# Performance work log

Measured on AMD Instinct MI355X. Metric: run time of the kernel, lower is better.

Reference implementation:

```python
import jax, jax.numpy as jnp
import numpy as np

jax.config.update("jax_enable_x64", True)

HLB_LVL_MAX = 20
HLB_LVL = 5
HLB_SHIFT = True
HLB_MAX = 2 ** HLB_LVL_MAX                      # 1048576
HLB_BIAS = (2 ** (HLB_LVL_MAX - HLB_LVL) - 1) if HLB_SHIFT else 0   # 32767
NUM_BITS = HLB_LVL_MAX + (1 if HLB_SHIFT else 0)  # 21 bits per axis, 63 total -> int64


def hilbert_encode3d(grd, num_bits):
    """Skilling's AxesToTranspose + bit interleave: 3D grid coords -> Hilbert order.
    grd: [..., 3] int64, coords < 2**num_bits. Returns int64 [...].
    Fixed-trip-count Python loops over bits (unrolled at trace time, ~21 iters)."""
    nd = 3
    x = [grd[..., i] for i in range(nd)]
    M = 1 << (num_bits - 1)
    # Inverse undo excess work
    Q = M
    while Q > 1:
        P = Q - 1
        for i in range(nd):
            cond = (x[i] & Q) != 0
            t = (x[0] ^ x[i]) & P
            new_x0 = jnp.where(cond, x[0] ^ P, x[0] ^ t)   # invert low bits of x0, or exchange
            new_xi = jnp.where(cond, x[i], x[i] ^ t)
            x[0] = new_x0
            if i != 0:
                x[i] = new_xi
        Q >>= 1
    # Gray encode
    for i in range(1, nd):
        x[i] = x[i] ^ x[i - 1]
    t = jnp.zeros_like(x[0])
    Q = M
    while Q > 1:
        t = jnp.where((x[nd - 1] & Q) != 0, t ^ (Q - 1), t)
        Q >>= 1
    for i in range(nd):
        x[i] = x[i] ^ t
    # Interleave bits of the transposed coords (x[0] most significant at each level)
    h = jnp.zeros_like(x[0])
    for b in range(num_bits):
        for i in range(nd):
            bit = (x[i] >> b) & 1
            h = h | (bit << (b * nd + (nd - 1 - i)))
    return h


def setup_inputs() -> dict:
    key = jax.random.key(0)
    z = jax.random.normal(key, (32, 131072, 3), dtype=jnp.float32)
    return {"z": z}


def reference(z):
    z = z.astype(jnp.float64)
    z_ce = z.mean(axis=1, keepdims=True)                                  # [B,1,3]
    r = jnp.sqrt(jnp.max(jnp.sum((z - z_ce) ** 2, axis=2), axis=1))       # [B]
    z_r = r[:, None, None] + 1e-6                                          # [B,1,1]
    z_nm = (z - z_ce + z_r) / (2.0 * z_r)                                  # normalized to ~[0,1]
    grd_idx = (HLB_MAX * z_nm).astype(jnp.int64) + HLB_BIAS                # quantize (trunc toward 0)
    hlb_ord = hilbert_encode3d(grd_idx, NUM_BITS)                          # [B,N] int64
    idx_pa = jnp.argsort(hlb_ord, axis=1)                                  # permutation along curve
    idx_re = jnp.argsort(idx_pa, axis=1)                                   # inverse permutation
    return idx_pa, idx_re
```

## Files before the change

kernel.cpp:

```cpp
#include <hip/hip_runtime.h>

typedef unsigned int u32;
typedef unsigned long long u64;
typedef unsigned short u16;

#define NB 32
#define NP 131072
#define THREADS 256
#define STHREADS 512
#define RADIX 256
#define PASSES 6

#define SBPB 32
#define STILE 4096
#define SIPT 8
#define EBPB 64
#define ETILE 2048
#define EIPT 8



__device__ __forceinline__ u64 spread3(u32 v) {
    u64 x = (u64)(v & 0x1FFFFFu);
    x = (x | (x << 32)) & 0x001F00000000FFFFull;
    x = (x | (x << 16)) & 0x001F0000FF0000FFull;
    x = (x | (x << 8))  & 0x100F00F00F00F00Full;
    x = (x | (x << 4))  & 0x10C30C30C30C30C3ull;
    x = (x | (x << 2))  & 0x1249249249249249ull;
    return x;
}

__device__ __forceinline__ u64 hilbert3d(u32 x0, u32 x1, u32 x2) {
    #pragma unroll
    for (int q = 20; q >= 3; --q) {
        u32 Q = 1u << q, P = Q - 1u;
        if (x0 & Q) x0 ^= P;
        u32 t = (x0 ^ x1) & P;
        if (x1 & Q) { x0 ^= P; } else { x0 ^= t; x1 ^= t; }
        t = (x0 ^ x2) & P;
        if (x2 & Q) { x0 ^= P; } else { x0 ^= t; x2 ^= t; }
    }
    x1 ^= x0;
    x2 ^= x1;
    u32 y = x2;
    y ^= y >> 1; y ^= y >> 2; y ^= y >> 4; y ^= y >> 8; y ^= y >> 16;
    u32 t2 = y >> 1;
    x0 ^= t2; x1 ^= t2; x2 ^= t2;
    return (spread3(x0) << 2) | (spread3(x1) << 1) | spread3(x2);
}


__global__ __launch_bounds__(THREADS) void k_sum(const float* __restrict__ z,
                                                 double* __restrict__ partial) {
    int id = blockIdx.x;
    int b = (id & 7) * 4 + ((id >> 3) >> 6);
    int blk = (id >> 3) & 63;
    int tid = threadIdx.x;
    const float* zb = z + ((size_t)b * NP + (size_t)blk * ETILE) * 3;
    double s0 = 0.0, s1 = 0.0, s2 = 0.0;
    #pragma unroll
    for (int r = 0; r < EIPT; ++r) {
        int p = r * THREADS + tid;
        s0 += (double)zb[p * 3 + 0];
        s1 += (double)zb[p * 3 + 1];
        s2 += (double)zb[p * 3 + 2];
    }
    for (int off = 32; off > 0; off >>= 1) {
        s0 += __shfl_down(s0, off);
        s1 += __shfl_down(s1, off);
        s2 += __shfl_down(s2, off);
    }
    __shared__ double red[4][3];
    int lane = tid & 63, wave = tid >> 6;
    if (lane == 0) { red[wave][0] = s0; red[wave][1] = s1; red[wave][2] = s2; }
    __syncthreads();
    if (tid == 0) {
        size_t o = ((size_t)b * EBPB + blk) * 3;
        partial[o + 0] = red[0][0] + red[1][0] + red[2][0] + red[3][0];
        partial[o + 1] = red[0][1] + red[1][1] + red[2][1] + red[3][1];
        partial[o + 2] = red[0][2] + red[1][2] + red[2][2] + red[3][2];
    }
}

__global__ __launch_bounds__(64) void k_centroid(const double* __restrict__ partial,
                                                 double* __restrict__ cent) {
    int b = blockIdx.x, lane = threadIdx.x;
    size_t o = ((size_t)b * EBPB + lane) * 3;
    double v0 = partial[o + 0], v1 = partial[o + 1], v2 = partial[o + 2];
    for (int off = 32; off > 0; off >>= 1) {
        v0 += __shfl_down(v0, off);
        v1 += __shfl_down(v1, off);
        v2 += __shfl_down(v2, off);
    }
    if (lane == 0) {
        cent[b * 4 + 0] = v0 / (double)NP;
        cent[b * 4 + 1] = v1 / (double)NP;
        cent[b * 4 + 2] = v2 / (double)NP;
    }
}

__global__ __launch_bounds__(THREADS) void k_maxp(const float* __restrict__ z,
                                                  const double* __restrict__ cent,
                                                  double* __restrict__ pmax) {
    int id = blockIdx.x;
    int b = (id & 7) * 4 + ((id >> 3) >> 6);
    int blk = (id >> 3) & 63;
    int tid = threadIdx.x;
    double c0 = cent[b * 4 + 0], c1 = cent[b * 4 + 1], c2 = cent[b * 4 + 2];
    const float* zb = z + ((size_t)b * NP + (size_t)blk * ETILE) * 3;
    double m = 0.0;
    #pragma unroll
    for (int r = 0; r < EIPT; ++r) {
        int p = r * THREADS + tid;
        double d0 = (double)zb[p * 3 + 0] - c0;
        double d1 = (double)zb[p * 3 + 1] - c1;
        double d2 = (double)zb[p * 3 + 2] - c2;
        double s = (d0 * d0 + d1 * d1) + d2 * d2;
        m = fmax(m, s);
    }
    for (int off = 32; off > 0; off >>= 1) m = fmax(m, __shfl_down(m, off));
    __shared__ double red[4];
    int lane = tid & 63, wave = tid >> 6;
    if (lane == 0) red[wave] = m;
    __syncthreads();
    if (tid == 0) pmax[(size_t)b * EBPB + blk] = fmax(fmax(red[0], red[1]), fmax(red[2], red[3]));
}

__global__ __launch_bounds__(64) void k_radius(const double* __restrict__ pmax,
                                               const double* __restrict__ cent,
                                               double* __restrict__ norm) {
    int b = blockIdx.x, lane = threadIdx.x;
    double m = pmax[(size_t)b * EBPB + lane];
    for (int off = 32; off > 0; off >>= 1) m = fmax(m, __shfl_down(m, off));
    if (lane == 0) {
        double zr = sqrt(m) + 1e-6;
        double A = 1048576.0 / (2.0 * zr);
        norm[b * 4 + 0] = A;
        norm[b * 4 + 1] = (zr - cent[b * 4 + 0]) * A;
        norm[b * 4 + 2] = (zr - cent[b * 4 + 1]) * A;
        norm[b * 4 + 3] = (zr - cent[b * 4 + 2]) * A;
    }
}


__global__ __launch_bounds__(THREADS) void k_encode(const float* __restrict__ z,
                                                    const double* __restrict__ norm,
                                                    u32* __restrict__ klo,
                                                    u32* __restrict__ khi,
                                                    u32* __restrict__ hist) {
    int id = blockIdx.x;
    int b = (id & 7) * 4 + ((id >> 3) >> 6);
    int blk = (id >> 3) & 63;
    int tid = threadIdx.x;
    __shared__ u32 lh[RADIX];
    lh[tid] = 0;
    __syncthreads();
    double A  = norm[b * 4 + 0];
    double B0 = norm[b * 4 + 1], B1 = norm[b * 4 + 2], B2 = norm[b * 4 + 3];
    size_t batchBase = (size_t)b * NP;
    for (int r = 0; r < EIPT; ++r) {
        int p = blk * ETILE + r * THREADS + tid;
        size_t zi = (batchBase + p) * 3;
        u32 g0 = (u32)fma((double)z[zi + 0], A, B0) + 32767u;
        u32 g1 = (u32)fma((double)z[zi + 1], A, B1) + 32767u;
        u32 g2 = (u32)fma((double)z[zi + 2], A, B2) + 32767u;
        u64 key = hilbert3d(g0, g1, g2) >> 16;
        u32 lo = (u32)key;
        u32 hp = ((u32)(key >> 32) << 17) | (u32)p;
        klo[batchBase + p] = lo;
        khi[batchBase + p] = hp;
        atomicAdd(&lh[lo & 255u], 1u);
    }
    __syncthreads();
    hist[((size_t)b * RADIX + tid) * EBPB + blk] = lh[tid];
}

__device__ u32 g_lut[128];

__global__ __launch_bounds__(THREADS) void k_encode2(const float* __restrict__ z,
                                                     const double* __restrict__ norm,
                                                     u32* __restrict__ klo,
                                                     u32* __restrict__ khi,
                                                     u32* __restrict__ hist) {
    int id = blockIdx.x;
    int b = (id & 7) * 4 + ((id >> 3) >> 6);
    int blk = (id >> 3) & 63;
    int tid = threadIdx.x;
    __shared__ u32 lh[RADIX];
    __shared__ u32 ltw[128];
    lh[tid] = 0;
    if (tid < 128) ltw[tid] = g_lut[tid];
    __syncthreads();
    const unsigned char* lt = (const unsigned char*)ltw;
    double A  = norm[b * 4 + 0];
    double B0 = norm[b * 4 + 1], B1 = norm[b * 4 + 2], B2 = norm[b * 4 + 3];
    size_t batchBase = (size_t)b * NP;
    #pragma unroll
    for (int rr = 0; rr < EIPT; rr += 4) {
        u32 g0[4], g1[4], g2[4];
        #pragma unroll
        for (int j = 0; j < 4; ++j) {
            int p = blk * ETILE + (rr + j) * THREADS + tid;
            size_t zi = (batchBase + p) * 3;
            g0[j] = (u32)fma((double)z[zi + 0], A, B0) + 32767u;
            g1[j] = (u32)fma((double)z[zi + 1], A, B1) + 32767u;
            g2[j] = (u32)fma((double)z[zi + 2], A, B2) + 32767u;
        }
        u32 st[4] = {0u, 0u, 0u, 0u};
        u32 Hh[4] = {0u, 0u, 0u, 0u};
        u32 Hl[4] = {0u, 0u, 0u, 0u};
        #pragma unroll
        for (int l = 20; l >= 12; --l) {
            #pragma unroll
            for (int j = 0; j < 4; ++j) {
                u32 o = (((g0[j] >> l) & 1u) << 2) | (((g1[j] >> l) & 1u) << 1)
                      | ((g2[j] >> l) & 1u);
                u32 e = (u32)lt[st[j] | o];
                Hh[j] = (Hh[j] << 3) | (e & 7u);
                st[j] = e & 0xF8u;
            }
        }
        #pragma unroll
        for (int l = 11; l >= 2; --l) {
            #pragma unroll
            for (int j = 0; j < 4; ++j) {
                u32 o = (((g0[j] >> l) & 1u) << 2) | (((g1[j] >> l) & 1u) << 1)
                      | ((g2[j] >> l) & 1u);
                u32 e = (u32)lt[st[j] | o];
                Hl[j] = (Hl[j] << 3) | (e & 7u);
                st[j] = e & 0xF8u;
            }
        }
        #pragma unroll
        for (int j = 0; j < 4; ++j) {
            int p = blk * ETILE + (rr + j) * THREADS + tid;
            u32 lo = (Hl[j] >> 10) | (Hh[j] << 20);
            u32 hp = ((Hh[j] >> 12) << 17) | (u32)p;
            klo[batchBase + p] = lo;
            khi[batchBase + p] = hp;
            atomicAdd(&lh[lo & 255u], 1u);
        }
    }
    __syncthreads();
    hist[((size_t)b * RADIX + tid) * EBPB + blk] = lh[tid];
}


__global__ __launch_bounds__(THREADS) void k_hist(const u32* __restrict__ dig,
                                                  u32* __restrict__ hist, int shift) {
    int id = blockIdx.x;
    int b = (id & 7) * 4 + ((id >> 3) >> 6);
    int blk = (id >> 3) & 63;
    int tid = threadIdx.x;
    __shared__ u32 lh[RADIX];
    lh[tid] = 0;
    __syncthreads();
    const uint4* dv = (const uint4*)(dig + (size_t)b * NP + (size_t)blk * ETILE);
    #pragma unroll
    for (int r = 0; r < EIPT / 4; ++r) {
        uint4 k = dv[r * THREADS + tid];
        atomicAdd(&lh[(k.x >> shift) & 255u], 1u);
        atomicAdd(&lh[(k.y >> shift) & 255u], 1u);
        atomicAdd(&lh[(k.z >> shift) & 255u], 1u);
        atomicAdd(&lh[(k.w >> shift) & 255u], 1u);
    }
    __syncthreads();
    hist[((size_t)b * RADIX + tid) * EBPB + blk] = lh[tid];
}


template<bool HAS_W1, bool OUT_W0, bool LAST>
__global__ __launch_bounds__(STHREADS, 8) void k_scatter(
    const u32* __restrict__ digIn,
    const u32* __restrict__ w1In,
    u32* __restrict__ w0Out, u32* __restrict__ w1Out,
    int* __restrict__ out0, int* __restrict__ out1,
    const u32* __restrict__ hist, int shiftW)
{
    int id = blockIdx.x;
    int b = (id & 7) * 4 + ((id >> 3) >> 5);
    int blk = (id >> 3) & 31;
    int tid = threadIdx.x, lane = tid & 63, wave = tid >> 6;

    __shared__ __align__(16) u32 sbuf[HAS_W1 ? 2 * STILE : STILE];
    __shared__ u16 wrun[8][RADIX];
    __shared__ u16 lstart[RADIX];
    __shared__ u32 baseS[RADIX];
    __shared__ u32 wsum[4];
    uint2* stage2 = reinterpret_cast<uint2*>(sbuf);
    u32* stage1 = sbuf;

    {
        int d2 = tid & 255, hw = (tid >> 8) * 4;
        wrun[hw + 0][d2] = 0; wrun[hw + 1][d2] = 0;
        wrun[hw + 2][d2] = 0; wrun[hw + 3][d2] = 0;
    }

    size_t batchBase = (size_t)b * NP;
    u32 tileOff = (u32)blk * STILE + (u32)wave * (STILE / 8);

    u32 w0[SIPT], w1v[SIPT], dr[SIPT];
    u64 lmask = (1ull << lane) - 1ull;

    #pragma unroll
    for (int it = 0; it < SIPT; ++it)
        w0[it] = digIn[batchBase + tileOff + it * 64 + lane];
    if (HAS_W1) {
        #pragma unroll
        for (int it = 0; it < SIPT; ++it)
            w1v[it] = w1In[batchBase + tileOff + it * 64 + lane];
    }

    u32 tot = 0, part = 0, vscan = 0;
    if (tid < 256) {
        const uint4* hp = (const uint4*)(hist + ((size_t)b * RADIX + tid) * EBPB);
        int lim = blk * 2;
        #pragma unroll
        for (int q = 0; q < EBPB / 4; ++q) {
            uint4 v = hp[q];
            int s = q * 4;
            tot += v.x + v.y + v.z + v.w;
            part += (s + 0 < lim ? v.x : 0u) + (s + 1 < lim ? v.y : 0u)
                  + (s + 2 < lim ? v.z : 0u) + (s + 3 < lim ? v.w : 0u);
        }
        vscan = tot;
        for (int off = 1; off < 64; off <<= 1) {
            u32 n = __shfl_up(vscan, off);
            if (lane >= off) vscan += n;
        }
        if (lane == 63) wsum[wave] = vscan;
    }
    __syncthreads();
    if (tid < 256) {
        u32 woff = 0;
        for (int w = 0; w < 4; ++w)
            if (w < wave) woff += wsum[w];
        baseS[tid] = woff + vscan - tot + part;
    }

    #pragma unroll
    for (int it = 0; it < SIPT; ++it) {
        u32 d = (w0[it] >> shiftW) & 255u;
        u64 m = ~0ull;
        #pragma unroll
        for (int bb = 0; bb < 8; ++bb) {
            u64 bal = __ballot((d >> bb) & 1u);
            m &= ((d >> bb) & 1u) ? bal : ~bal;
        }
        u32 lower = (u32)__popcll(m & lmask);
        u32 base = (u32)wrun[wave][d];
        if (lower == 0) wrun[wave][d] = (u16)(base + (u32)__popcll(m));
        dr[it] = (d << 16) | (base + lower);
    }
    __syncthreads();

    u32 cnt = 0, vs2 = 0;
    if (tid < 256) {
        u32 run = 0;
        #pragma unroll
        for (int w = 0; w < 8; ++w) { u32 c = wrun[w][tid]; wrun[w][tid] = (u16)run; run += c; }
        cnt = run;
        vs2 = cnt;
        for (int off = 1; off < 64; off <<= 1) {
            u32 n = __shfl_up(vs2, off);
            if (lane >= off) vs2 += n;
        }
        if (lane == 63) wsum[wave] = vs2;
    }
    __syncthreads();
    if (tid < 256) {
        u32 woff = 0;
        for (int w = 0; w < 4; ++w)
            if (w < wave) woff += wsum[w];
        lstart[tid] = (u16)(woff + vs2 - cnt);
    }
    __syncthreads();

    if (HAS_W1) {
        #pragma unroll
        for (int it = 0; it < SIPT; ++it) {
            u32 d = dr[it] >> 16, r = dr[it] & 0xFFFFu;
            u32 slot = (u32)lstart[d] + (u32)wrun[wave][d] + r;
            stage2[slot] = make_uint2(w0[it], w1v[it]);
        }
        __syncthreads();
        #pragma unroll
        for (int r = 0; r < SIPT; ++r) {
            int s = r * STHREADS + tid;
            uint2 kv = stage2[s];
            u32 d = (kv.x >> shiftW) & 255u;
            u32 pos = baseS[d] + (u32)s - (u32)lstart[d];
            if (OUT_W0) w0Out[batchBase + pos] = kv.x;
            w1Out[batchBase + pos] = kv.y;
        }
    } else {
        #pragma unroll
        for (int it = 0; it < SIPT; ++it) {
            u32 d = dr[it] >> 16, r = dr[it] & 0xFFFFu;
            u32 slot = (u32)lstart[d] + (u32)wrun[wave][d] + r;
            stage1[slot] = w0[it];
        }
        __syncthreads();
        #pragma unroll
        for (int r = 0; r < SIPT; ++r) {
            int s = r * STHREADS + tid;
            u32 k = stage1[s];
            u32 d = (k >> shiftW) & 255u;
            u32 pos = baseS[d] + (u32)s - (u32)lstart[d];
            if (LAST) {
                u32 idx = k & 0x1FFFFu;
                out0[batchBase + pos] = (int)idx;
                out1[batchBase + idx] = (int)pos;
            } else {
                w0Out[batchBase + pos] = k;
            }
        }
    }
}


namespace lut_build {

static u64 hfull(u32 a, u32 bcoord, u32 c) {
    u32 x[3] = {a, bcoord, c};
    const u32 M = 1u << 20;
    for (u32 Q = M; Q > 1; Q >>= 1) {
        u32 P = Q - 1u;
        for (int i = 0; i < 3; ++i) {
            if (x[i] & Q) x[0] ^= P;
            else { u32 t = (x[0] ^ x[i]) & P; x[0] ^= t; x[i] ^= t; }
        }
    }
    x[1] ^= x[0]; x[2] ^= x[1];
    u32 t = 0;
    for (u32 Q = M; Q > 1; Q >>= 1) if (x[2] & Q) t ^= (Q - 1u);
    x[0] ^= t; x[1] ^= t; x[2] ^= t;
    u64 h = 0;
    for (int bb = 0; bb < 21; ++bb)
        for (int i = 0; i < 3; ++i)
            h |= (u64)((x[i] >> bb) & 1u) << (bb * 3 + (2 - i));
    return h;
}

static int digit_at(u32 p0, u32 p1, u32 p2, int l) {
    return (int)((hfull(p0, p1, p2) >> (3 * l)) & 7u);
}

struct Sig { unsigned char v[72]; };

static bool sig_eq(const Sig& x, const Sig& y) {
    for (int i = 0; i < 72; ++i) if (x.v[i] != y.v[i]) return false;
    return true;
}

static void mk_sig(u32 c0, u32 c1, u32 c2, int l, Sig& s) {
    for (int o = 0; o < 8; ++o) {
        u32 p0 = c0 | ((u32)((o >> 2) & 1) << l);
        u32 p1 = c1 | ((u32)((o >> 1) & 1) << l);
        u32 p2 = c2 | ((u32)(o & 1) << l);
        s.v[o] = (unsigned char)digit_at(p0, p1, p2, l);
        for (int o2 = 0; o2 < 8; ++o2) {
            u32 q0 = p0 | ((u32)((o2 >> 2) & 1) << (l - 1));
            u32 q1 = p1 | ((u32)((o2 >> 1) & 1) << (l - 1));
            u32 q2 = p2 | ((u32)(o2 & 1) << (l - 1));
            s.v[8 + o * 8 + o2] = (unsigned char)digit_at(q0, q1, q2, l - 1);
        }
    }
}

static bool build(unsigned char* tab) {
    const int MAXS = 48;
    static Sig sigs[MAXS];
    struct Node { u32 c0, c1, c2; int l; };
    static Node nodes[MAXS];
    bool expanded[MAXS] = {false};
    int ns = 0;
    for (int i = 0; i < 512; ++i) tab[i] = 0;
    mk_sig(0, 0, 0, 20, sigs[0]);
    nodes[0] = {0, 0, 0, 20};
    ns = 1;
    bool progress = true;
    while (progress) {
        progress = false;
        for (int sI = 0; sI < ns; ++sI) {
            if (expanded[sI]) continue;
            Node n = nodes[sI];
            if (n.l < 2) return false;
            for (int o = 0; o < 8; ++o) {
                u32 p0 = n.c0 | ((u32)((o >> 2) & 1) << n.l);
                u32 p1 = n.c1 | ((u32)((o >> 1) & 1) << n.l);
                u32 p2 = n.c2 | ((u32)(o & 1) << n.l);
                int d = digit_at(p0, p1, p2, n.l);
                Sig cs; mk_sig(p0, p1, p2, n.l - 1, cs);
                int cid = -1;
                for (int k = 0; k < ns; ++k)
                    if (sig_eq(sigs[k], cs)) { cid = k; break; }
                if (cid < 0) {
                    if (ns >= MAXS) return false;
                    cid = ns;
                    sigs[ns] = cs;
                    nodes[ns] = {p0, p1, p2, n.l - 1};
                    ns++;
                }
                if (cid >= 32) return false;
                tab[sI * 8 + o] = (unsigned char)(d | (cid << 3));
            }
            expanded[sI] = true;
            progress = true;
        }
    }
    u64 rng = 0x9E3779B97F4A7C15ull;
    for (int it = 0; it < 6008; ++it) {
        u32 p0, p1, p2;
        if (it < 8) {
            p0 = (it & 4) ? 0x1FFFFFu : 0u;
            p1 = (it & 2) ? 0x1FFFFFu : 0u;
            p2 = (it & 1) ? 0x1FFFFFu : 0u;
        } else {
            rng ^= rng << 13; rng ^= rng >> 7; rng ^= rng << 17; p0 = (u32)(rng & 0x1FFFFFu);
            rng ^= rng << 13; rng ^= rng >> 7; rng ^= rng << 17; p1 = (u32)(rng & 0x1FFFFFu);
            rng ^= rng << 13; rng ^= rng >> 7; rng ^= rng << 17; p2 = (u32)(rng & 0x1FFFFFu);
        }
        u32 s8 = 0, Hh = 0, Hl = 0;
        for (int l = 20; l >= 12; --l) {
            u32 o = (((p0 >> l) & 1u) << 2) | (((p1 >> l) & 1u) << 1) | ((p2 >> l) & 1u);
            u32 e = tab[s8 | o];
            Hh = (Hh << 3) | (e & 7u);
            s8 = e & 0xF8u;
        }
        for (int l = 11; l >= 2; --l) {
            u32 o = (((p0 >> l) & 1u) << 2) | (((p1 >> l) & 1u) << 1) | ((p2 >> l) & 1u);
            u32 e = tab[s8 | o];
            Hl = (Hl << 3) | (e & 7u);
            s8 = e & 0xF8u;
        }
        u32 lo = (Hl >> 10) | (Hh << 20);
        u32 hi15 = Hh >> 12;
        u64 key = ((u64)hi15 << 32) | (u64)lo;
        if (key != (hfull(p0, p1, p2) >> 16)) return false;
    }
    return true;
}

}

static unsigned char h_tab[512];

struct LutInit {
    bool ok;
    void* dev;
    LutInit() : ok(false), dev(nullptr) {
        ok = lut_build::build(h_tab);
        if (ok) {
            if (hipGetSymbolAddress(&dev, HIP_SYMBOL(g_lut)) != hipSuccess || dev == nullptr)
                ok = false;
        }
    }
};


extern "C" void kernel_launch(void* const* d_in, const int* in_sizes, int n_in,
                              void* d_out, int out_size, void* d_ws, size_t ws_size,
                              hipStream_t stream) {
    const float* z = (const float*)d_in[0];
    int* out0 = (int*)d_out;
    int* out1 = out0 + (size_t)NB * NP;

    char* ws = (char*)d_ws;
    u32* loA  = (u32*)(ws + 0);
    u32* hiA  = (u32*)(ws + 16777216);
    u32* loB  = (u32*)(ws + 33554432);
    u32* hiB  = (u32*)(ws + 50331648);
    u32* hist = (u32*)(ws + 67108864);
    double* partial = (double*)(ws + 69206016);
    double* pmax    = (double*)(ws + 69255168);
    double* cent    = (double*)(ws + 69271552);
    double* norm    = (double*)(ws + 69272576);

    static LutInit li;

    const int egrid = NB * EBPB;
    const int sgrid = NB * SBPB;

    if (li.ok) {
        hipMemcpyAsync(li.dev, h_tab, 512, hipMemcpyHostToDevice, stream);
    }

    k_sum<<<egrid, THREADS, 0, stream>>>(z, partial);
    k_centroid<<<NB, 64, 0, stream>>>(partial, cent);
    k_maxp<<<egrid, THREADS, 0, stream>>>(z, cent, pmax);
    k_radius<<<NB, 64, 0, stream>>>(pmax, cent, norm);
    if (li.ok) {
        k_encode2<<<egrid, THREADS, 0, stream>>>(z, norm, loA, hiA, hist);
    } else {
        k_encode<<<egrid, THREADS, 0, stream>>>(z, norm, loA, hiA, hist);
    }

    k_scatter<true,  true,  false><<<sgrid, STHREADS, 0, stream>>>(
        loA, hiA, loB, hiB, nullptr, nullptr, hist, 0);
    k_hist<<<egrid, THREADS, 0, stream>>>(loB, hist, 8);
    k_scatter<true,  true,  false><<<sgrid, STHREADS, 0, stream>>>(
        loB, hiB, loA, hiA, nullptr, nullptr, hist, 8);
    k_hist<<<egrid, THREADS, 0, stream>>>(loA, hist, 16);
    k_scatter<true,  true,  false><<<sgrid, STHREADS, 0, stream>>>(
        loA, hiA, loB, hiB, nullptr, nullptr, hist, 16);
    k_hist<<<egrid, THREADS, 0, stream>>>(loB, hist, 24);
    k_scatter<true,  false, false><<<sgrid, STHREADS, 0, stream>>>(
        loB, hiB, nullptr, hiA, nullptr, nullptr, hist, 24);
    k_hist<<<egrid, THREADS, 0, stream>>>(hiA, hist, 17);
    k_scatter<false, true,  false><<<sgrid, STHREADS, 0, stream>>>(
        hiA, nullptr, hiB, nullptr, nullptr, nullptr, hist, 17);
    k_hist<<<egrid, THREADS, 0, stream>>>(hiB, hist, 25);
    k_scatter<false, false, true ><<<sgrid, STHREADS, 0, stream>>>(
        hiB, nullptr, nullptr, nullptr, out0, out1, hist, 25);
}
```

Measured before the change: 307.8 us.

## Fold centroid and radius reductions into consumers; vectorize z loads and key stores

Removes the two tiny single-wave kernels (k_centroid, k_radius). Each block of k_maxp and k_encode now recomputes the per-batch centroid and normalization from the partial sums and partial maxima in a shared-memory prologue. The z reads in k_maxp and k_encode2 switch to float4 loads that cover four points per thread, and the key stores become uint4. This saves two launches and their serialization gaps, plus some memory transactions, at the cost of redundant small reductions in every block and a different point-to-thread mapping.

```diff
diff --git a/kernel.cpp b/kernel.cpp
--- a/kernel.cpp
+++ b/kernel.cpp
@@ -11,13 +11,13 @@
 #define RADIX 256
 #define PASSES 6
 
+
 #define SBPB 32
 #define STILE 4096
 #define SIPT 8
 #define EBPB 64
 #define ETILE 2048
 #define EIPT 8
-
 
 
 __device__ __forceinline__ u64 spread3(u32 v) {
@@ -82,41 +82,47 @@
     }
 }
 
-__global__ __launch_bounds__(64) void k_centroid(const double* __restrict__ partial,
-                                                 double* __restrict__ cent) {
-    int b = blockIdx.x, lane = threadIdx.x;
-    size_t o = ((size_t)b * EBPB + lane) * 3;
-    double v0 = partial[o + 0], v1 = partial[o + 1], v2 = partial[o + 2];
-    for (int off = 32; off > 0; off >>= 1) {
-        v0 += __shfl_down(v0, off);
-        v1 += __shfl_down(v1, off);
-        v2 += __shfl_down(v2, off);
-    }
-    if (lane == 0) {
-        cent[b * 4 + 0] = v0 / (double)NP;
-        cent[b * 4 + 1] = v1 / (double)NP;
-        cent[b * 4 + 2] = v2 / (double)NP;
-    }
-}
-
 __global__ __launch_bounds__(THREADS) void k_maxp(const float* __restrict__ z,
-                                                  const double* __restrict__ cent,
+                                                  const double* __restrict__ partial,
                                                   double* __restrict__ pmax) {
     int id = blockIdx.x;
     int b = (id & 7) * 4 + ((id >> 3) >> 6);
     int blk = (id >> 3) & 63;
     int tid = threadIdx.x;
-    double c0 = cent[b * 4 + 0], c1 = cent[b * 4 + 1], c2 = cent[b * 4 + 2];
-    const float* zb = z + ((size_t)b * NP + (size_t)blk * ETILE) * 3;
+    __shared__ double cS[3];
+    if (tid < 64) {
+        size_t o = ((size_t)b * EBPB + tid) * 3;
+        double v0 = partial[o + 0], v1 = partial[o + 1], v2 = partial[o + 2];
+        for (int off = 32; off > 0; off >>= 1) {
+            v0 += __shfl_down(v0, off);
+            v1 += __shfl_down(v1, off);
+            v2 += __shfl_down(v2, off);
+        }
+        if (tid == 0) {
+            cS[0] = v0 / (double)NP;
+            cS[1] = v1 / (double)NP;
+            cS[2] = v2 / (double)NP;
+        }
+    }
+    __syncthreads();
+    double c0 = cS[0], c1 = cS[1], c2 = cS[2];
+    const float4* zb4 = (const float4*)(z + ((size_t)b * NP + (size_t)blk * ETILE) * 3);
     double m = 0.0;
     #pragma unroll
-    for (int r = 0; r < EIPT; ++r) {
-        int p = r * THREADS + tid;
-        double d0 = (double)zb[p * 3 + 0] - c0;
-        double d1 = (double)zb[p * 3 + 1] - c1;
-        double d2 = (double)zb[p * 3 + 2] - c2;
-        double s = (d0 * d0 + d1 * d1) + d2 * d2;
-        m = fmax(m, s);
+    for (int g = 0; g < 2; ++g) {
+        int q4 = g * 768 + tid * 3;
+        float4 va = zb4[q4 + 0], vb = zb4[q4 + 1], vc = zb4[q4 + 2];
+        float px[4] = {va.x, va.w, vb.z, vc.y};
+        float py[4] = {va.y, vb.x, vb.w, vc.z};
+        float pz[4] = {va.z, vb.y, vc.x, vc.w};
+        #pragma unroll
+        for (int j = 0; j < 4; ++j) {
+            double d0 = (double)px[j] - c0;
+            double d1 = (double)py[j] - c1;
+            double d2 = (double)pz[j] - c2;
+            double s = (d0 * d0 + d1 * d1) + d2 * d2;
+            m = fmax(m, s);
+        }
     }
     for (int off = 32; off > 0; off >>= 1) m = fmax(m, __shfl_down(m, off));
     __shared__ double red[4];
@@ -126,25 +132,34 @@
     if (tid == 0) pmax[(size_t)b * EBPB + blk] = fmax(fmax(red[0], red[1]), fmax(red[2], red[3]));
 }
 
-__global__ __launch_bounds__(64) void k_radius(const double* __restrict__ pmax,
-                                               const double* __restrict__ cent,
-                                               double* __restrict__ norm) {
-    int b = blockIdx.x, lane = threadIdx.x;
-    double m = pmax[(size_t)b * EBPB + lane];
-    for (int off = 32; off > 0; off >>= 1) m = fmax(m, __shfl_down(m, off));
-    if (lane == 0) {
-        double zr = sqrt(m) + 1e-6;
-        double A = 1048576.0 / (2.0 * zr);
-        norm[b * 4 + 0] = A;
-        norm[b * 4 + 1] = (zr - cent[b * 4 + 0]) * A;
-        norm[b * 4 + 2] = (zr - cent[b * 4 + 1]) * A;
-        norm[b * 4 + 3] = (zr - cent[b * 4 + 2]) * A;
-    }
-}
-
+
+__device__ __forceinline__ void quant_prologue(const double* __restrict__ partial,
+                                               const double* __restrict__ pmax,
+                                               int b, int tid, double* nS) {
+    if (tid < 64) {
+        size_t o = ((size_t)b * EBPB + tid) * 3;
+        double v0 = partial[o + 0], v1 = partial[o + 1], v2 = partial[o + 2];
+        for (int off = 32; off > 0; off >>= 1) {
+            v0 += __shfl_down(v0, off);
+            v1 += __shfl_down(v1, off);
+            v2 += __shfl_down(v2, off);
+        }
+        double m = pmax[(size_t)b * EBPB + tid];
+        for (int off = 32; off > 0; off >>= 1) m = fmax(m, __shfl_down(m, off));
+        if (tid == 0) {
+            double zr = sqrt(m) + 1e-6;
+            double A = 1048576.0 / (2.0 * zr);
+            nS[0] = A;
+            nS[1] = (zr - v0 / (double)NP) * A;
+            nS[2] = (zr - v1 / (double)NP) * A;
+            nS[3] = (zr - v2 / (double)NP) * A;
+        }
+    }
+}
 
 __global__ __launch_bounds__(THREADS) void k_encode(const float* __restrict__ z,
-                                                    const double* __restrict__ norm,
+                                                    const double* __restrict__ partial,
+                                                    const double* __restrict__ pmax,
                                                     u32* __restrict__ klo,
                                                     u32* __restrict__ khi,
                                                     u32* __restrict__ hist) {
@@ -153,10 +168,11 @@
     int blk = (id >> 3) & 63;
     int tid = threadIdx.x;
     __shared__ u32 lh[RADIX];
+    __shared__ double nS[4];
     lh[tid] = 0;
-    __syncthreads();
-    double A  = norm[b * 4 + 0];
-    double B0 = norm[b * 4 + 1], B1 = norm[b * 4 + 2], B2 = norm[b * 4 + 3];
+    quant_prologue(partial, pmax, b, tid, nS);
+    __syncthreads();
+    double A = nS[0], B0 = nS[1], B1 = nS[2], B2 = nS[3];
     size_t batchBase = (size_t)b * NP;
     for (int r = 0; r < EIPT; ++r) {
         int p = blk * ETILE + r * THREADS + tid;
@@ -178,7 +194,8 @@
 __device__ u32 g_lut[128];
 
 __global__ __launch_bounds__(THREADS) void k_encode2(const float* __restrict__ z,
-                                                     const double* __restrict__ norm,
+                                                     const double* __restrict__ partial,
+                                                     const double* __restrict__ pmax,
                                                      u32* __restrict__ klo,
                                                      u32* __restrict__ khi,
                                                      u32* __restrict__ hist) {
@@ -188,23 +205,29 @@
     int tid = threadIdx.x;
     __shared__ u32 lh[RADIX];
     __shared__ u32 ltw[128];
+    __shared__ double nS[4];
     lh[tid] = 0;
-    if (tid < 128) ltw[tid] = g_lut[tid];
+    if (tid >= 128 && tid < 256) ltw[tid - 128] = g_lut[tid - 128];
+    quant_prologue(partial, pmax, b, tid, nS);
     __syncthreads();
     const unsigned char* lt = (const unsigned char*)ltw;
-    double A  = norm[b * 4 + 0];
-    double B0 = norm[b * 4 + 1], B1 = norm[b * 4 + 2], B2 = norm[b * 4 + 3];
+    double A = nS[0], B0 = nS[1], B1 = nS[2], B2 = nS[3];
     size_t batchBase = (size_t)b * NP;
+    const float4* zb4 = (const float4*)(z + (batchBase + (size_t)blk * ETILE) * 3);
     #pragma unroll
-    for (int rr = 0; rr < EIPT; rr += 4) {
+    for (int g = 0; g < 2; ++g) {
+        int p0i = blk * ETILE + g * 1024 + tid * 4;
+        int q4 = g * 768 + tid * 3;
+        float4 va = zb4[q4 + 0], vb = zb4[q4 + 1], vc = zb4[q4 + 2];
+        float px[4] = {va.x, va.w, vb.z, vc.y};
+        float py[4] = {va.y, vb.x, vb.w, vc.z};
+        float pz[4] = {va.z, vb.y, vc.x, vc.w};
         u32 g0[4], g1[4], g2[4];
         #pragma unroll
         for (int j = 0; j < 4; ++j) {
-            int p = blk * ETILE + (rr + j) * THREADS + tid;
-            size_t zi = (batchBase + p) * 3;
-            g0[j] = (u32)fma((double)z[zi + 0], A, B0) + 32767u;
-            g1[j] = (u32)fma((double)z[zi + 1], A, B1) + 32767u;
-            g2[j] = (u32)fma((double)z[zi + 2], A, B2) + 32767u;
+            g0[j] = (u32)fma((double)px[j], A, B0) + 32767u;
+            g1[j] = (u32)fma((double)py[j], A, B1) + 32767u;
+            g2[j] = (u32)fma((double)pz[j], A, B2) + 32767u;
         }
         u32 st[4] = {0u, 0u, 0u, 0u};
         u32 Hh[4] = {0u, 0u, 0u, 0u};
@@ -231,15 +254,15 @@
                 st[j] = e & 0xF8u;
             }
         }
+        u32 lo[4], hp[4];
         #pragma unroll
         for (int j = 0; j < 4; ++j) {
-            int p = blk * ETILE + (rr + j) * THREADS + tid;
-            u32 lo = (Hl[j] >> 10) | (Hh[j] << 20);
-            u32 hp = ((Hh[j] >> 12) << 17) | (u32)p;
-            klo[batchBase + p] = lo;
-            khi[batchBase + p] = hp;
-            atomicAdd(&lh[lo & 255u], 1u);
-        }
+            lo[j] = (Hl[j] >> 10) | (Hh[j] << 20);
+            hp[j] = ((Hh[j] >> 12) << 17) | (u32)(p0i + j);
+            atomicAdd(&lh[lo[j] & 255u], 1u);
+        }
+        *(uint4*)(klo + batchBase + p0i) = make_uint4(lo[0], lo[1], lo[2], lo[3]);
+        *(uint4*)(khi + batchBase + p0i) = make_uint4(hp[0], hp[1], hp[2], hp[3]);
     }
     __syncthreads();
     hist[((size_t)b * RADIX + tid) * EBPB + blk] = lh[tid];
@@ -574,8 +597,6 @@
     u32* hist = (u32*)(ws + 67108864);
     double* partial = (double*)(ws + 69206016);
     double* pmax    = (double*)(ws + 69255168);
-    double* cent    = (double*)(ws + 69271552);
-    double* norm    = (double*)(ws + 69272576);
 
     static LutInit li;
 
@@ -587,13 +608,11 @@
     }
 
     k_sum<<<egrid, THREADS, 0, stream>>>(z, partial);
-    k_centroid<<<NB, 64, 0, stream>>>(partial, cent);
-    k_maxp<<<egrid, THREADS, 0, stream>>>(z, cent, pmax);
-    k_radius<<<NB, 64, 0, stream>>>(pmax, cent, norm);
+    k_maxp<<<egrid, THREADS, 0, stream>>>(z, partial, pmax);
     if (li.ok) {
-        k_encode2<<<egrid, THREADS, 0, stream>>>(z, norm, loA, hiA, hist);
+        k_encode2<<<egrid, THREADS, 0, stream>>>(z, partial, pmax, loA, hiA, hist);
     } else {
-        k_encode<<<egrid, THREADS, 0, stream>>>(z, norm, loA, hiA, hist);
+        k_encode<<<egrid, THREADS, 0, stream>>>(z, partial, pmax, loA, hiA, hist);
     }
 
     k_scatter<true,  true,  false><<<sgrid, STHREADS, 0, stream>>>(
```

Measured after the change: 306.4 us. No clear change (-0.5%).
